# Performance work log

Hardware: AMD Instinct MI355X
Metric: run time of the kernel (lower is better)

Reference implementation:

```python
import jax, jax.numpy as jnp
import numpy as np

N = 1000000
SH_COEFFS = 16  # (sh_degree+1)^2 with sh_degree=3
H = 256
W = 256
K_RENDER = 1000  # module renders min(1000, N) front-most-by-descending-depth splats


def setup_inputs():
    key = jax.random.key(0)
    k = jax.random.split(key, 5)
    positions = jax.random.normal(k[0], (N, 3), jnp.float32) * 0.1
    scales = jnp.ones((N, 3), jnp.float32) * 0.01
    rotations = jax.random.normal(k[1], (N, 4), jnp.float32)
    colors = jax.random.normal(k[2], (N, 3), jnp.float32)
    opacity = jnp.ones((N, 1), jnp.float32) * 0.1
    colors_sh = jax.random.normal(k[3], (N, SH_COEFFS, 3), jnp.float32) * 0.001
    # realistic pinhole camera: fx=fy=500, cx=cy=128, translation z=2 so depths>0
    camera_matrix = jnp.array([[500.0, 0.0, 128.0, 0.0],
                               [0.0, 500.0, 128.0, 0.0],
                               [0.0, 0.0, 1.0, 2.0]], jnp.float32)
    camera_position = jax.random.normal(k[4], (3,), jnp.float32) * 0.1
    return {"positions": positions, "scales": scales, "rotations": rotations,
            "colors": colors, "opacity": opacity, "colors_sh": colors_sh,
            "camera_matrix": camera_matrix, "camera_position": camera_position,
            "image_height": H, "image_width": W}


def _covariance(scales, rotations):
    # Sigma = R S S^T R^T, quaternion -> rotation matrix
    q = rotations / jnp.linalg.norm(rotations, axis=-1, keepdims=True)
    w, x, y, z = q[:, 0], q[:, 1], q[:, 2], q[:, 3]
    R = jnp.stack([
        jnp.stack([1 - 2 * (y * y + z * z), 2 * (x * y - w * z), 2 * (x * z + w * y)], -1),
        jnp.stack([2 * (x * y + w * z), 1 - 2 * (x * x + z * z), 2 * (y * z - w * x)], -1),
        jnp.stack([2 * (x * z - w * y), 2 * (y * z + w * x), 1 - 2 * (x * x + y * y)], -1)], -2)  # [N,3,3]
    s2 = jnp.clip(scales, 1e-7, None) ** 2
    return jnp.einsum('nij,nj,nkj->nik', R, s2, R)


def _sh_bases(d):
    x, y, z = d[:, 0], d[:, 1], d[:, 2]
    return jnp.stack([
        jnp.full_like(x, 0.28209479177387814),
        -0.48860251190291987 * y, 0.48860251190291987 * z, -0.48860251190291987 * x,
        1.0925484305920792 * x * y, -1.0925484305920792 * y * z,
        0.31539156525252005 * (2 * z * z - x * x - y * y),
        -1.0925484305920792 * x * z, 0.5462742152960396 * (x * x - y * y)], -1)  # [N,9]


def _forward(positions, scales, rotations, colors, opacity, colors_sh,
             camera_matrix, camera_position, image_height, image_width):
    cov3d = _covariance(jnp.exp(scales), rotations)  # [N,3,3]
    # perspective projection
    pos_h = jnp.concatenate([positions, jnp.ones((positions.shape[0], 1), positions.dtype)], -1)
    proj = pos_h @ camera_matrix.T  # [N,3]
    depths = proj[:, 2]
    pos2d = proj[:, :2] / (depths[:, None] + 1e-7)
    fx, fy = camera_matrix[0, 0], camera_matrix[1, 1]
    zero = jnp.zeros_like(depths)
    J = jnp.stack([
        jnp.stack([fx / depths, zero, -fx * pos2d[:, 0] / depths], -1),
        jnp.stack([zero, fy / depths, -fy * pos2d[:, 1] / depths], -1)], -2)  # [N,2,3]
    cov2d = jnp.einsum('nij,njk,nlk->nil', J, cov3d, J)  # [N,2,2]
    # view-dependent color via SH (only first 9 bases, as in the torch loop)
    vd = positions - camera_position[None]
    vd = vd / jnp.linalg.norm(vd, axis=-1, keepdims=True)
    sh = _sh_bases(vd)
    col = jax.nn.sigmoid(colors + jnp.einsum('nkc,nk->nc', colors_sh[:, :sh.shape[-1]], sh))
    op = jax.nn.sigmoid(opacity[:, 0])
    # depth sort descending, keep first K_RENDER (matches min(1000, N) loop)
    order = jnp.argsort(-depths)[:K_RENDER]
    mu_s, cov_s, col_s, op_s = pos2d[order], cov2d[order], col[order], op[order]
    ys = jnp.arange(image_height, dtype=jnp.float32)
    xs = jnp.arange(image_width, dtype=jnp.float32)
    yy, xx = jnp.meshgrid(ys, xs, indexing='ij')
    px = xx.reshape(-1)
    py = yy.reshape(-1)  # [P]
    P = image_height * image_width

    def step(carry, g):
        rendered, acc = carry
        mu, cv, c, o = g
        # 2x2 inverse of (cov + 1e-6 I), closed form
        a = cv[0, 0] + 1e-6
        b = cv[0, 1]
        cc = cv[1, 0]
        d = cv[1, 1] + 1e-6
        det = a * d - b * cc
        dx = px - mu[0]
        dy = py - mu[1]
        qv = (d * dx * dx - (b + cc) * dx * dy + a * dy * dy) / det
        alpha = o * jnp.exp(-0.5 * qv)           # [P]
        contrib = (1.0 - acc) * alpha            # front-to-back compositing
        rendered = rendered + contrib[:, None] * c
        acc = acc + contrib
        return (rendered, acc), None

    init = (jnp.zeros((P, 3), jnp.float32), jnp.zeros((P,), jnp.float32))
    (rendered, _), _ = jax.lax.scan(step, init, (mu_s, cov_s, col_s, op_s))
    return rendered.reshape(image_height, image_width, 3)


def reference(positions, scales, rotations, colors, opacity, colors_sh,
              camera_matrix, camera_position, image_height, image_width):
    return _forward(positions, scales, rotations, colors, opacity, colors_sh,
                    camera_matrix, camera_position, image_height, image_width)
```

## Files before the change

### kernel.cpp

```cpp
#include <hip/hip_runtime.h>
#include <stdint.h>

typedef uint32_t u32;
typedef uint64_t u64;

#define KREN 1000
#define NBLK 256
#define NTHR 1024
#define TOT (NBLK * NTHR)
#define CAND_CAP 4096
#define GSTRIDE 12
#define SEGN 4
#define KPER (KREN / SEGN)

__device__ __forceinline__ u32 fkey(float f) {
  u32 b = __float_as_uint(f);
  return (b & 0x80000000u) ? ~b : (b | 0x80000000u);
}

__device__ __forceinline__ void grid_sync(u32* bar) {
  __syncthreads();
  if (threadIdx.x == 0) {
    u32 gen = __hip_atomic_load(&bar[1], __ATOMIC_RELAXED, __HIP_MEMORY_SCOPE_AGENT);
    u32 arr = __hip_atomic_fetch_add(&bar[0], 1u, __ATOMIC_RELEASE, __HIP_MEMORY_SCOPE_AGENT);
    if (arr == NBLK - 1) {
      __hip_atomic_store(&bar[0], 0u, __ATOMIC_RELAXED, __HIP_MEMORY_SCOPE_AGENT);
      __hip_atomic_store(&bar[1], gen + 1u, __ATOMIC_RELEASE, __HIP_MEMORY_SCOPE_AGENT);
    } else {
      while (__hip_atomic_load(&bar[1], __ATOMIC_RELAXED, __HIP_MEMORY_SCOPE_AGENT) == gen)
        __builtin_amdgcn_s_sleep(4);
    }
    __builtin_amdgcn_fence(__ATOMIC_ACQUIRE, "agent");
  }
  __syncthreads();
}

__device__ __forceinline__ void pick_scan(const u32* __restrict__ hist, u32 K,
                                          u32* lds, int* bin_out, u32* Krem_out) {
  int tid = threadIdx.x;
  u32 hv[4];
  u32 s = 0;
#pragma unroll
  for (int k = 0; k < 4; ++k) { hv[k] = hist[tid * 4 + k]; s += hv[k]; }
  lds[tid] = s;
  __syncthreads();
  for (int d = 1; d < NTHR; d <<= 1) {
    u32 v = lds[tid] + ((tid + d < NTHR) ? lds[tid + d] : 0u);
    __syncthreads();
    lds[tid] = v;
    __syncthreads();
  }
  u32 inc = lds[tid];
  u32 above = (tid < NTHR - 1) ? lds[tid + 1] : 0u;
  if (above < K && inc >= K) {
    u32 cum = above;
    for (int k = 3; k >= 0; --k) {
      cum += hv[k];
      if (cum >= K) {
        lds[NTHR] = (u32)(tid * 4 + k);
        lds[NTHR + 1] = K - (cum - hv[k]);
        break;
      }
    }
  }
  __syncthreads();
  *bin_out = (int)lds[NTHR];
  *Krem_out = lds[NTHR + 1];
  __syncthreads();
}

__global__ __launch_bounds__(NTHR) void k_fused(
    const float* __restrict__ pos, const float* __restrict__ scales,
    const float* __restrict__ rot, const float* __restrict__ colors,
    const float* __restrict__ opac, const float* __restrict__ csh,
    const float* __restrict__ cam, const float* __restrict__ campos,
    u32* __restrict__ keys, u64* __restrict__ cand, float* __restrict__ gauss,
    u32* __restrict__ hist1, u32* __restrict__ hist2, u32* __restrict__ state,
    u32* __restrict__ bar, float* __restrict__ out, int N, int shstride) {
  __shared__ u64 smem[8192];
  u32* hl = (u32*)smem;
  int tid = threadIdx.x, bid = blockIdx.x;
  int gtid = bid * NTHR + tid;

  for (int i = tid; i < 4096; i += NTHR) hl[i] = 0;
  __syncthreads();
  {
    float c8 = cam[8], c9 = cam[9], c10 = cam[10], c11 = cam[11];
    for (int i = gtid; i < N; i += TOT) {
      float x = pos[3 * i], y = pos[3 * i + 1], z = pos[3 * i + 2];
      u32 mk = fkey(c8 * x + c9 * y + c10 * z + c11);
      keys[i] = mk;
      u32 bin = mk >> 20;
      u64 todo = __ballot(true);
      while (todo) {
        int leader = __ffsll((unsigned long long)todo) - 1;
        u32 lbin = __shfl(bin, leader, 64);
        u64 same = __ballot(bin == lbin);
        if ((int)(tid & 63) == leader) atomicAdd(&hl[lbin], (u32)__popcll(same & todo));
        todo &= ~same;
      }
    }
  }
  __syncthreads();
  for (int i = tid; i < 4096; i += NTHR) {
    u32 v = hl[i];
    if (v) atomicAdd(&hist1[i], v);
  }
  grid_sync(bar);

  int bin1; u32 K1;
  pick_scan(hist1, (u32)KREN, hl, &bin1, &K1);
  u32 pref = (u32)bin1;
  for (int i = tid; i < 4096; i += NTHR) hl[i] = 0;
  __syncthreads();
  for (int i = gtid; i < N; i += TOT) {
    u32 k = keys[i];
    if ((k >> 20) == pref) atomicAdd(&hl[(k >> 8) & 4095u], 1u);
  }
  __syncthreads();
  for (int i = tid; i < 4096; i += NTHR) {
    u32 v = hl[i];
    if (v) atomicAdd(&hist2[i], v);
  }
  grid_sync(bar);

  int bin2; u32 K2;
  pick_scan(hist2, K1, hl, &bin2, &K2);
  {
    u32 T = (pref << 20) | (((u32)bin2) << 8);
    for (int i = gtid; i < N; i += TOT) {
      u32 k = keys[i];
      if (k >= T) {
        u32 p = atomicAdd(&state[0], 1u);
        if (p < CAND_CAP) cand[p] = (((u64)(~k)) << 32) | (u32)i;
      }
    }
  }
  grid_sync(bar);

  if (bid < CAND_CAP / NTHR) {
    u64* s = smem;
    int M = (int)state[0];
    if (M > CAND_CAP) M = CAND_CAP;
    for (int i = tid; i < M; i += NTHR) s[i] = cand[i];
    __syncthreads();
    int i = gtid;
    if (i < M) {
      u64 mine = s[i];
      int r = 0;
      for (int j = 0; j < M; ++j) r += (s[j] < mine) ? 1 : 0;
      if (r < KREN) {
        int g = (int)(u32)(mine & 0xffffffffu);
        float x = pos[3 * g], y = pos[3 * g + 1], z = pos[3 * g + 2];
        float c0 = cam[0], c1 = cam[1], c2 = cam[2], c3 = cam[3];
        float c4 = cam[4], c5 = cam[5], c6 = cam[6], c7 = cam[7];
        float c8 = cam[8], c9 = cam[9], c10 = cam[10], c11 = cam[11];
        float dep = c8 * x + c9 * y + c10 * z + c11;
        float invd = 1.0f / (dep + 1e-7f);
        float p2x = (c0 * x + c1 * y + c2 * z + c3) * invd;
        float p2y = (c4 * x + c5 * y + c6 * z + c7) * invd;
        float qw = rot[4 * g], qx = rot[4 * g + 1], qy = rot[4 * g + 2], qz = rot[4 * g + 3];
        float qn = rsqrtf(qw * qw + qx * qx + qy * qy + qz * qz);
        qw *= qn; qx *= qn; qy *= qn; qz *= qn;
        float r00 = 1.f - 2.f * (qy * qy + qz * qz), r01 = 2.f * (qx * qy - qw * qz), r02 = 2.f * (qx * qz + qw * qy);
        float r10 = 2.f * (qx * qy + qw * qz), r11 = 1.f - 2.f * (qx * qx + qz * qz), r12 = 2.f * (qy * qz - qw * qx);
        float r20 = 2.f * (qx * qz - qw * qy), r21 = 2.f * (qy * qz + qw * qx), r22 = 1.f - 2.f * (qx * qx + qy * qy);
        float e0 = fmaxf(expf(scales[3 * g]), 1e-7f);
        float e1 = fmaxf(expf(scales[3 * g + 1]), 1e-7f);
        float e2 = fmaxf(expf(scales[3 * g + 2]), 1e-7f);
        float v0 = e0 * e0, v1 = e1 * e1, v2 = e2 * e2;
        float C00 = r00 * r00 * v0 + r01 * r01 * v1 + r02 * r02 * v2;
        float C01 = r00 * r10 * v0 + r01 * r11 * v1 + r02 * r12 * v2;
        float C02 = r00 * r20 * v0 + r01 * r21 * v1 + r02 * r22 * v2;
        float C11 = r10 * r10 * v0 + r11 * r11 * v1 + r12 * r12 * v2;
        float C12 = r10 * r20 * v0 + r11 * r21 * v1 + r12 * r22 * v2;
        float C22 = r20 * r20 * v0 + r21 * r21 * v1 + r22 * r22 * v2;
        float fx = c0, fy = c5;
        float jd = 1.0f / dep;
        float j0 = fx * jd, j2 = -fx * p2x * jd, j4 = fy * jd, j5 = -fy * p2y * jd;
        float u0x = j0 * C00 + j2 * C02;
        float u0y = j0 * C01 + j2 * C12;
        float u0z = j0 * C02 + j2 * C22;
        float u1y = j4 * C11 + j5 * C12;
        float u1z = j4 * C12 + j5 * C22;
        float a = u0x * j0 + u0z * j2 + 1e-6f;
        float b = u0y * j4 + u0z * j5;
        float d2 = u1y * j4 + u1z * j5 + 1e-6f;
        float det = a * d2 - b * b;
        float idet = 1.0f / det;
        const float L = 1.4426950408889634f;
        float Aq = -0.5f * L * d2 * idet;
        float Bq = L * b * idet;
        float Cq = -0.5f * L * a * idet;
        float vx = x - campos[0], vy = y - campos[1], vz = z - campos[2];
        float vn = rsqrtf(vx * vx + vy * vy + vz * vz);
        vx *= vn; vy *= vn; vz *= vn;
        float sh[9];
        sh[0] = 0.28209479177387814f;
        sh[1] = -0.48860251190291987f * vy;
        sh[2] = 0.48860251190291987f * vz;
        sh[3] = -0.48860251190291987f * vx;
        sh[4] = 1.0925484305920792f * vx * vy;
        sh[5] = -1.0925484305920792f * vy * vz;
        sh[6] = 0.31539156525252005f * (2.f * vz * vz - vx * vx - vy * vy);
        sh[7] = -1.0925484305920792f * vx * vz;
        sh[8] = 0.5462742152960396f * (vx * vx - vy * vy);
        float col[3];
        for (int c = 0; c < 3; ++c) {
          float accv = colors[3 * g + c];
          for (int k2 = 0; k2 < 9; ++k2) accv += sh[k2] * csh[(size_t)g * shstride + 3 * k2 + c];
          col[c] = 1.0f / (1.0f + __expf(-accv));
        }
        float op = 1.0f / (1.0f + __expf(-opac[g]));
        float* G = gauss + r * GSTRIDE;
        G[0] = p2x; G[1] = p2y; G[2] = Aq; G[3] = Bq; G[4] = Cq;
        G[5] = op;  G[6] = col[0]; G[7] = col[1]; G[8] = col[2];
        G[9] = 0.f; G[10] = 0.f; G[11] = 0.f;
      }
    }
  }
  grid_sync(bar);

  {
    float* gs = (float*)smem;
    float* comb = gs + 12000;
    for (int i = tid; i < KREN * GSTRIDE; i += NTHR) gs[i] = gauss[i];
    __syncthreads();
    int q = tid & 255;
    int seg = tid >> 8;
    int p = bid * 256 + q;
    float px = (float)(p & 255);
    float py = (float)(p >> 8);
    float cr = 0.f, cg = 0.f, cb = 0.f, acc = 0.f;
    int k0 = seg * KPER;
    for (int k = k0; k < k0 + KPER; ++k) {
      const float4* G = (const float4*)(gs + k * GSTRIDE);
      float4 g0 = G[0];
      float4 g1 = G[1];
      float g2x = gs[k * GSTRIDE + 8];
      float dx = px - g0.x, dy = py - g0.y;
      float sE = g0.z * dx * dx + g0.w * dx * dy + g1.x * dy * dy;
      float alpha = g1.y * exp2f(sE);
      float w = (1.0f - acc) * alpha;
      cr += w * g1.z; cg += w * g1.w; cb += w * g2x;
      acc += w;
    }
    comb[tid * 4 + 0] = cr;
    comb[tid * 4 + 1] = cg;
    comb[tid * 4 + 2] = cb;
    comb[tid * 4 + 3] = 1.0f - acc;
    __syncthreads();
    if (tid < 256) {
      float R = 0.f, Gc = 0.f, B = 0.f, T = 1.f;
#pragma unroll
      for (int s2 = 0; s2 < SEGN; ++s2) {
        int idx = (s2 * 256 + tid) * 4;
        R += T * comb[idx + 0];
        Gc += T * comb[idx + 1];
        B += T * comb[idx + 2];
        T *= comb[idx + 3];
      }
      out[3 * p + 0] = R;
      out[3 * p + 1] = Gc;
      out[3 * p + 2] = B;
    }
  }
}

extern "C" void kernel_launch(void* const* d_in, const int* in_sizes, int n_in,
                              void* d_out, int out_size, void* d_ws, size_t ws_size,
                              hipStream_t stream) {
  const float* positions = (const float*)d_in[0];
  const float* scales    = (const float*)d_in[1];
  const float* rotations = (const float*)d_in[2];
  const float* colors    = (const float*)d_in[3];
  const float* opacity   = (const float*)d_in[4];
  const float* colors_sh = (const float*)d_in[5];
  const float* cam       = (const float*)d_in[6];
  const float* campos    = (const float*)d_in[7];
  int N = in_sizes[0] / 3;
  int shstride = in_sizes[5] / N;

  char* ws = (char*)d_ws;
  u32* keys    = (u32*)ws;
  u64* cand    = (u64*)(ws + 4194304);
  float* gauss = (float*)(ws + 4227072);
  char* zr     = ws + 4276224;
  u32* hist1   = (u32*)zr;
  u32* hist2   = (u32*)(zr + 16384);
  u32* state   = (u32*)(zr + 32768);
  u32* bar     = (u32*)(zr + 33024);
  float* out   = (float*)d_out;

  hipMemsetAsync(zr, 0, 33280, stream);

  void* args[] = {(void*)&positions, (void*)&scales, (void*)&rotations, (void*)&colors,
                  (void*)&opacity, (void*)&colors_sh, (void*)&cam, (void*)&campos,
                  (void*)&keys, (void*)&cand, (void*)&gauss,
                  (void*)&hist1, (void*)&hist2, (void*)&state, (void*)&bar,
                  (void*)&out, (void*)&N, (void*)&shstride};
  hipLaunchCooperativeKernel((const void*)k_fused, dim3(NBLK), dim3(NTHR), args, 0, stream);
}
```

Measured before the change: 448.6 us.

## Compact top-bin candidates early, wave-parallel ranking, 4-pixel render with 16 segments

During the second histogram pass, keys that fall in the selected top bin are appended to a compact candidate buffer with wave-aggregated atomics. The third pass then scans that small buffer instead of rereading all N keys. Candidate ranking is spread over all blocks, one wavefront per candidate, with a shuffle reduction, and only lane 0 preprocesses the gaussian. The renderer now gives each thread 4 horizontally adjacent pixels, computing their quadratic forms incrementally, and splits the gaussians into 16 depth segments that are composited at the end. The risks are a silent overflow if the top bin holds more than 16384 entries, and extra exp2 work per thread plus higher register pressure.

```diff
diff --git a/kernel.cpp b/kernel.cpp
--- a/kernel.cpp
+++ b/kernel.cpp
@@ -8,10 +8,11 @@
 #define NBLK 256
 #define NTHR 1024
 #define TOT (NBLK * NTHR)
+#define CAND0_CAP 16384
 #define CAND_CAP 4096
 #define GSTRIDE 12
-#define SEGN 4
-#define KPER (KREN / SEGN)
+#define SEGN 16
+#define PXT 4
 
 __device__ __forceinline__ u32 fkey(float f) {
   u32 b = __float_as_uint(f);
@@ -74,13 +75,15 @@
     const float* __restrict__ rot, const float* __restrict__ colors,
     const float* __restrict__ opac, const float* __restrict__ csh,
     const float* __restrict__ cam, const float* __restrict__ campos,
-    u32* __restrict__ keys, u64* __restrict__ cand, float* __restrict__ gauss,
-    u32* __restrict__ hist1, u32* __restrict__ hist2, u32* __restrict__ state,
-    u32* __restrict__ bar, float* __restrict__ out, int N, int shstride) {
+    u32* __restrict__ keys, u64* __restrict__ cand0, u64* __restrict__ cand,
+    float* __restrict__ gauss, u32* __restrict__ hist1, u32* __restrict__ hist2,
+    u32* __restrict__ state, u32* __restrict__ bar, float* __restrict__ out,
+    int N, int shstride) {
   __shared__ u64 smem[8192];
   u32* hl = (u32*)smem;
   int tid = threadIdx.x, bid = blockIdx.x;
   int gtid = bid * NTHR + tid;
+  int lane = tid & 63;
 
   for (int i = tid; i < 4096; i += NTHR) hl[i] = 0;
   __syncthreads();
@@ -96,7 +99,7 @@
         int leader = __ffsll((unsigned long long)todo) - 1;
         u32 lbin = __shfl(bin, leader, 64);
         u64 same = __ballot(bin == lbin);
-        if ((int)(tid & 63) == leader) atomicAdd(&hl[lbin], (u32)__popcll(same & todo));
+        if (lane == leader) atomicAdd(&hl[lbin], (u32)__popcll(same & todo));
         todo &= ~same;
       }
     }
@@ -115,7 +118,19 @@
   __syncthreads();
   for (int i = gtid; i < N; i += TOT) {
     u32 k = keys[i];
-    if ((k >> 20) == pref) atomicAdd(&hl[(k >> 8) & 4095u], 1u);
+    bool m = (k >> 20) == pref;
+    if (m) atomicAdd(&hl[(k >> 8) & 4095u], 1u);
+    u64 bm = __ballot(m);
+    if (bm) {
+      u32 base;
+      int leader = __ffsll((unsigned long long)bm) - 1;
+      if (lane == leader) base = atomicAdd(&state[1], (u32)__popcll(bm));
+      base = __shfl(base, leader, 64);
+      if (m) {
+        u32 p = base + (u32)__popcll(bm & ((1ull << lane) - 1ull));
+        if (p < CAND0_CAP) cand0[p] = (((u64)(~k)) << 32) | (u32)i;
+      }
+    }
   }
   __syncthreads();
   for (int i = tid; i < 4096; i += NTHR) {
@@ -127,29 +142,39 @@
   int bin2; u32 K2;
   pick_scan(hist2, K1, hl, &bin2, &K2);
   {
-    u32 T = (pref << 20) | (((u32)bin2) << 8);
-    for (int i = gtid; i < N; i += TOT) {
-      u32 k = keys[i];
-      if (k >= T) {
+    u32 Thi = ~((pref << 20) | (((u32)bin2) << 8));
+    int M1 = (int)state[1];
+    if (M1 > CAND0_CAP) M1 = CAND0_CAP;
+    for (int i = gtid; i < M1; i += TOT) {
+      u64 e = cand0[i];
+      if ((u32)(e >> 32) <= Thi) {
         u32 p = atomicAdd(&state[0], 1u);
-        if (p < CAND_CAP) cand[p] = (((u64)(~k)) << 32) | (u32)i;
+        if (p < CAND_CAP) cand[p] = e;
       }
     }
   }
   grid_sync(bar);
 
-  if (bid < CAND_CAP / NTHR) {
-    u64* s = smem;
+  {
+    u64* sc = smem;
     int M = (int)state[0];
     if (M > CAND_CAP) M = CAND_CAP;
-    for (int i = tid; i < M; i += NTHR) s[i] = cand[i];
-    __syncthreads();
-    int i = gtid;
-    if (i < M) {
-      u64 mine = s[i];
-      int r = 0;
-      for (int j = 0; j < M; ++j) r += (s[j] < mine) ? 1 : 0;
-      if (r < KREN) {
+    for (int i = tid; i < M; i += NTHR) sc[i] = cand[i];
+    __syncthreads();
+    int w = tid >> 6;
+    int c = bid * 16 + w;
+    if (c < M) {
+      u64 mine = sc[c];
+      int cnt = 0;
+      int JJ = (M + 63) >> 6;
+      for (int jj = 0; jj < JJ; ++jj) {
+        int j = lane + (jj << 6);
+        if (j < M && sc[j] < mine) ++cnt;
+      }
+#pragma unroll
+      for (int d = 32; d; d >>= 1) cnt += __shfl_xor(cnt, d, 64);
+      int r = cnt;
+      if (r < KREN && lane == 0) {
         int g = (int)(u32)(mine & 0xffffffffu);
         float x = pos[3 * g], y = pos[3 * g + 1], z = pos[3 * g + 2];
         float c0 = cam[0], c1 = cam[1], c2 = cam[2], c3 = cam[3];
@@ -206,10 +231,10 @@
         sh[7] = -1.0925484305920792f * vx * vz;
         sh[8] = 0.5462742152960396f * (vx * vx - vy * vy);
         float col[3];
-        for (int c = 0; c < 3; ++c) {
-          float accv = colors[3 * g + c];
-          for (int k2 = 0; k2 < 9; ++k2) accv += sh[k2] * csh[(size_t)g * shstride + 3 * k2 + c];
-          col[c] = 1.0f / (1.0f + __expf(-accv));
+        for (int c2 = 0; c2 < 3; ++c2) {
+          float accv = colors[3 * g + c2];
+          for (int k2 = 0; k2 < 9; ++k2) accv += sh[k2] * csh[(size_t)g * shstride + 3 * k2 + c2];
+          col[c2] = 1.0f / (1.0f + __expf(-accv));
         }
         float op = 1.0f / (1.0f + __expf(-opac[g]));
         float* G = gauss + r * GSTRIDE;
@@ -223,46 +248,61 @@
 
   {
     float* gs = (float*)smem;
-    float* comb = gs + 12000;
-    for (int i = tid; i < KREN * GSTRIDE; i += NTHR) gs[i] = gauss[i];
-    __syncthreads();
-    int q = tid & 255;
-    int seg = tid >> 8;
-    int p = bid * 256 + q;
-    float px = (float)(p & 255);
-    float py = (float)(p >> 8);
-    float cr = 0.f, cg = 0.f, cb = 0.f, acc = 0.f;
-    int k0 = seg * KPER;
-    for (int k = k0; k < k0 + KPER; ++k) {
-      const float4* G = (const float4*)(gs + k * GSTRIDE);
-      float4 g0 = G[0];
-      float4 g1 = G[1];
+    float4* g4s = (float4*)smem;
+    const float4* g4 = (const float4*)gauss;
+    for (int i = tid; i < 3000; i += NTHR) g4s[i] = g4[i];
+    __syncthreads();
+    int grp = tid & 63;
+    int seg = tid >> 6;
+    float pxf = (float)(grp * 4);
+    float pyf = (float)bid;
+    float cr0 = 0.f, cr1 = 0.f, cr2 = 0.f, cr3 = 0.f;
+    float cg0 = 0.f, cg1 = 0.f, cg2 = 0.f, cg3 = 0.f;
+    float cb0 = 0.f, cb1 = 0.f, cb2 = 0.f, cb3 = 0.f;
+    float ac0 = 0.f, ac1 = 0.f, ac2 = 0.f, ac3 = 0.f;
+    int gbeg = (seg * KREN) / SEGN, gend = ((seg + 1) * KREN) / SEGN;
+    for (int k = gbeg; k < gend; ++k) {
+      const float4* Gp = (const float4*)(gs + k * GSTRIDE);
+      float4 g0 = Gp[0];
+      float4 g1 = Gp[1];
       float g2x = gs[k * GSTRIDE + 8];
-      float dx = px - g0.x, dy = py - g0.y;
-      float sE = g0.z * dx * dx + g0.w * dx * dy + g1.x * dy * dy;
-      float alpha = g1.y * exp2f(sE);
-      float w = (1.0f - acc) * alpha;
-      cr += w * g1.z; cg += w * g1.w; cb += w * g2x;
-      acc += w;
-    }
-    comb[tid * 4 + 0] = cr;
-    comb[tid * 4 + 1] = cg;
-    comb[tid * 4 + 2] = cb;
-    comb[tid * 4 + 3] = 1.0f - acc;
+      float A = g0.z, B = g0.w, C = g1.x, op = g1.y;
+      float dx = pxf - g0.x, dy = pyf - g0.y;
+      float q0 = (A * dx + B * dy) * dx + C * dy * dy;
+      float u = 2.f * A * dx + B * dy;
+      float q1 = q0 + u + A;
+      float q2 = q0 + 2.f * u + 4.f * A;
+      float q3 = q0 + 3.f * u + 9.f * A;
+      float e0 = op * exp2f(q0), e1 = op * exp2f(q1);
+      float e2 = op * exp2f(q2), e3 = op * exp2f(q3);
+      float w0 = (1.f - ac0) * e0, w1 = (1.f - ac1) * e1;
+      float w2 = (1.f - ac2) * e2, w3 = (1.f - ac3) * e3;
+      cr0 += w0 * g1.z; cg0 += w0 * g1.w; cb0 += w0 * g2x; ac0 += w0;
+      cr1 += w1 * g1.z; cg1 += w1 * g1.w; cb1 += w1 * g2x; ac1 += w1;
+      cr2 += w2 * g1.z; cg2 += w2 * g1.w; cb2 += w2 * g2x; ac2 += w2;
+      cr3 += w3 * g1.z; cg3 += w3 * g1.w; cb3 += w3 * g2x; ac3 += w3;
+    }
+    __syncthreads();
+    float4* comb = (float4*)smem;
+    int base = seg * 256 + grp * 4;
+    comb[base + 0] = make_float4(cr0, cg0, cb0, 1.f - ac0);
+    comb[base + 1] = make_float4(cr1, cg1, cb1, 1.f - ac1);
+    comb[base + 2] = make_float4(cr2, cg2, cb2, 1.f - ac2);
+    comb[base + 3] = make_float4(cr3, cg3, cb3, 1.f - ac3);
     __syncthreads();
     if (tid < 256) {
-      float R = 0.f, Gc = 0.f, B = 0.f, T = 1.f;
+      int px = tid;
+      float R = 0.f, Gc = 0.f, Bc = 0.f, T = 1.f;
 #pragma unroll
       for (int s2 = 0; s2 < SEGN; ++s2) {
-        int idx = (s2 * 256 + tid) * 4;
-        R += T * comb[idx + 0];
-        Gc += T * comb[idx + 1];
-        B += T * comb[idx + 2];
-        T *= comb[idx + 3];
-      }
+        float4 cv = comb[s2 * 256 + px];
+        R += T * cv.x; Gc += T * cv.y; Bc += T * cv.z;
+        T *= cv.w;
+      }
+      int p = bid * 256 + px;
       out[3 * p + 0] = R;
       out[3 * p + 1] = Gc;
-      out[3 * p + 2] = B;
+      out[3 * p + 2] = Bc;
     }
   }
 }
@@ -283,9 +323,10 @@
 
   char* ws = (char*)d_ws;
   u32* keys    = (u32*)ws;
-  u64* cand    = (u64*)(ws + 4194304);
-  float* gauss = (float*)(ws + 4227072);
-  char* zr     = ws + 4276224;
+  u64* cand0   = (u64*)(ws + 4194304);
+  u64* cand    = (u64*)(ws + 4325376);
+  float* gauss = (float*)(ws + 4358144);
+  char* zr     = ws + 4407296;
   u32* hist1   = (u32*)zr;
   u32* hist2   = (u32*)(zr + 16384);
   u32* state   = (u32*)(zr + 32768);
@@ -296,7 +337,7 @@
 
   void* args[] = {(void*)&positions, (void*)&scales, (void*)&rotations, (void*)&colors,
                   (void*)&opacity, (void*)&colors_sh, (void*)&cam, (void*)&campos,
-                  (void*)&keys, (void*)&cand, (void*)&gauss,
+                  (void*)&keys, (void*)&cand0, (void*)&cand, (void*)&gauss,
                   (void*)&hist1, (void*)&hist2, (void*)&state, (void*)&bar,
                   (void*)&out, (void*)&N, (void*)&shstride};
   hipLaunchCooperativeKernel((const void*)k_fused, dim3(NBLK), dim3(NTHR), args, 0, stream);
```

After: 450.2 us. No clear change (+0.4%).
